# Performance work log

Measured on AMD Instinct MI355X. Metric: run time of the kernel, lower is better.

The kernel has to match this reference:

```python
import jax, jax.numpy as jnp
import numpy as np

N_NODES = 50000
N_EDGES = 500000
D_IN, D_HID = 128, 256


def _add_self_loops(edge_index, n):
    loop = jnp.arange(n, dtype=edge_index.dtype)
    src = jnp.concatenate([edge_index[0], loop])
    dst = jnp.concatenate([edge_index[1], loop])
    return src, dst


def _gcn_layer(x, W, b, src, dst, dinv_sqrt, n):
    # x: [N, d_in] -> h: [N, d_out]
    h = x @ W
    # symmetric normalization D^{-1/2} (A+I) D^{-1/2}
    norm = dinv_sqrt[src] * dinv_sqrt[dst]          # [E+N]
    msg = h[src] * norm[:, None]                    # gather + scale
    agg = jax.ops.segment_sum(msg, dst, num_segments=n)  # scatter-add
    return agg + b


def setup_inputs() -> dict:
    key = jax.random.key(0)
    ks = jax.random.split(key, 8)
    x = jax.random.normal(ks[0], (N_NODES, D_IN), dtype=jnp.float32)
    edge_index = jax.random.randint(ks[1], (2, N_EDGES), 0, N_NODES, dtype=jnp.int64 if jax.config.read('jax_enable_x64') else jnp.int32)
    s = lambda fan_in: 1.0 / np.sqrt(fan_in)
    W1 = jax.random.uniform(ks[2], (D_IN, D_HID), jnp.float32, -s(D_IN), s(D_IN))
    b1 = jnp.zeros((D_HID,), jnp.float32)
    W2 = jax.random.uniform(ks[3], (D_HID, D_HID), jnp.float32, -s(D_HID), s(D_HID))
    b2 = jnp.zeros((D_HID,), jnp.float32)
    W3 = jax.random.uniform(ks[4], (D_HID, D_HID), jnp.float32, -s(D_HID), s(D_HID))
    b3 = jnp.zeros((D_HID,), jnp.float32)
    return {"x": x, "edge_index": edge_index, "W1": W1, "b1": b1,
            "W2": W2, "b2": b2, "W3": W3, "b3": b3}


def reference(x, edge_index, W1, b1, W2, b2, W3, b3):
    n = x.shape[0]
    src, dst = _add_self_loops(edge_index, n)
    # degree includes self loops (edge weight 1), as in torch_geometric GCNConv
    deg = jax.ops.segment_sum(jnp.ones_like(dst, dtype=x.dtype), dst, num_segments=n)
    dinv_sqrt = jnp.where(deg > 0, jax.lax.rsqrt(jnp.maximum(deg, 1e-12)), 0.0)
    h = jax.nn.relu(_gcn_layer(x, W1, b1, src, dst, dinv_sqrt, n))
    h = jax.nn.relu(_gcn_layer(h, W2, b2, src, dst, dinv_sqrt, n))
    h = _gcn_layer(h, W3, b3, src, dst, dinv_sqrt, n)
    return h
```

## Files before the change

### kernel.cpp

```cpp
#include <hip/hip_runtime.h>

#define NNODES 50000
#define NEDGES 500000
#define DIN 128
#define DHID 256
#define MPAD 50048
#define NI4 12500
#define NSB 49

typedef unsigned short u16;
typedef __attribute__((ext_vector_type(8))) _Float16 half8;
typedef __attribute__((ext_vector_type(4))) float f32x4;

__device__ __forceinline__ u16 f2h(float f) {
  union { _Float16 h; u16 u; } v; v.h = (_Float16)f; return v.u;
}
__device__ __forceinline__ float h2f(unsigned int u) {
  union { _Float16 h; u16 u; } v; v.u = (u16)u; return (float)v.h;
}

__global__ void k_zero_i32(int* __restrict__ p, int n) {
  int i = blockIdx.x * blockDim.x + threadIdx.x;
  if (i < n) p[i] = 0;
}

__global__ void k_hist(const int* __restrict__ dst, int* __restrict__ deg, int e) {
  int i = blockIdx.x * blockDim.x + threadIdx.x;
  if (i < e) atomicAdd(&deg[dst[i]], 1);
}

__global__ __launch_bounds__(256) void k_blocksum(const int* __restrict__ deg,
                                                  int* __restrict__ partials) {
  __shared__ int red[256];
  int tid = threadIdx.x;
  int t4 = blockIdx.x * 256 + tid;
  int sum = 0;
  if (t4 < NI4) {
    int4 v = ((const int4*)deg)[t4];
    sum = v.x + v.y + v.z + v.w;
  }
  red[tid] = sum;
  __syncthreads();
  for (int off = 128; off > 0; off >>= 1) {
    if (tid < off) red[tid] += red[tid + off];
    __syncthreads();
  }
  if (tid == 0) partials[blockIdx.x] = red[0];
}

__global__ __launch_bounds__(256) void k_scan2(int* __restrict__ deg,
                                               const int* __restrict__ partials,
                                               int* __restrict__ row_ptr,
                                               float* __restrict__ dinv) {
  __shared__ int sdata[256];
  __shared__ int sprefix;
  int tid = threadIdx.x, bid = blockIdx.x;
  int t4 = bid * 256 + tid;
  int4 v = make_int4(0, 0, 0, 0);
  if (t4 < NI4) v = ((const int4*)deg)[t4];
  int tsum = v.x + v.y + v.z + v.w;
  sdata[tid] = tsum;
  if (tid == 0) {
    int pre = 0;
    for (int b = 0; b < bid; ++b) pre += partials[b];
    sprefix = pre;
  }
  __syncthreads();
  for (int off = 1; off < 256; off <<= 1) {
    int val = (tid >= off) ? sdata[tid - off] : 0;
    __syncthreads();
    sdata[tid] += val;
    __syncthreads();
  }
  if (t4 < NI4) {
    int run = sdata[tid] - tsum + sprefix;
    int base = t4 * 4;
    float4 dv;
    dv.x = rsqrtf((float)v.x + 1.0f);
    dv.y = rsqrtf((float)v.y + 1.0f);
    dv.z = rsqrtf((float)v.z + 1.0f);
    dv.w = rsqrtf((float)v.w + 1.0f);
    *(float4*)(dinv + base) = dv;
    row_ptr[base + 0] = run; run += v.x;
    row_ptr[base + 1] = run; run += v.y;
    row_ptr[base + 2] = run; run += v.z;
    row_ptr[base + 3] = run; run += v.w;
    if (base + 4 == NNODES) row_ptr[NNODES] = run;
    ((int4*)deg)[t4] = make_int4(0, 0, 0, 0);
  }
}

__global__ void k_fill(const int* __restrict__ src, const int* __restrict__ dst,
                       const float* __restrict__ dinv, const int* __restrict__ row_ptr,
                       int* __restrict__ cursor, int* __restrict__ csr_src,
                       float* __restrict__ csr_nrm, int e) {
  int i = blockIdx.x * blockDim.x + threadIdx.x;
  if (i < e) {
    int d = dst[i], s = src[i];
    int pos = row_ptr[d] + atomicAdd(&cursor[d], 1);
    csr_src[pos] = s;
    csr_nrm[pos] = dinv[s] * dinv[d];
  }
}

__global__ void k_prep(const float* __restrict__ x, u16* __restrict__ xh, int total4,
                       const float* __restrict__ W1f, u16* __restrict__ P1,
                       const float* __restrict__ W2f, u16* __restrict__ P2,
                       const float* __restrict__ W3f, u16* __restrict__ P3) {
  int i = blockIdx.x * blockDim.x + threadIdx.x;
  if (i < total4) {
    float4 v = ((const float4*)x)[i];
    ushort4 o;
    o.x = f2h(v.x); o.y = f2h(v.y); o.z = f2h(v.z); o.w = f2h(v.w);
    ((ushort4*)xh)[i] = o;
  }
  const int s1 = DIN * 256, s2 = s1 + DHID * 256, s3 = s2 + DHID * 256;
  if (i < s3) {
    const float* W; u16* P; int li;
    if (i < s1)      { W = W1f; P = P1; li = i; }
    else if (i < s2) { W = W2f; P = P2; li = i - s1; }
    else             { W = W3f; P = P3; li = i - s2; }
    int k = li >> 8, n = li & 255;
    int t = k >> 5, q = (k >> 3) & 3, j = k & 7;
    int c = n >> 4, m = n & 15;
    int f = (c * 64 + q * 16 + m) * 8 + j;
    float w = W[li] * 256.0f;
    u16 hi = f2h(w);
    u16 lo = f2h(w - h2f(hi));
    P[(size_t)t * 16384 + f] = hi;
    P[(size_t)t * 16384 + 8192 + f] = lo;
  }
}

template<int K, int EPI>
__global__ __launch_bounds__(256, 6) void k_fused(const u16* __restrict__ hf,
                                                  const float* __restrict__ dinv,
                                                  const int* __restrict__ row_ptr,
                                                  const int* __restrict__ csr_src,
                                                  const float* __restrict__ csr_nrm,
                                                  const u16* __restrict__ Bpk,
                                                  const float* __restrict__ bias,
                                                  u16* __restrict__ hf16,
                                                  float* __restrict__ outf) {
  __shared__ __align__(16) u16 As[32 * K];

  {
    constexpr int GL = K / 8;
    constexpr int NGRP = 256 / GL;
    constexpr int RPG = 32 / NGRP;
    const int gg = threadIdx.x / GL;
    const int sub = threadIdx.x % GL;
    const int coff = sub * 8;
    const int nbase = blockIdx.x * 32;

    for (int k = 0; k < RPG; ++k) {
      const int row = gg + k * NGRP;
      const int node = nbase + row;
      float acc[8];
      if (node < NNODES) {
        float di = dinv[node];
        float s2 = di * di;
        {
          half8 v = *(const half8*)(hf + (size_t)node * K + coff);
#pragma unroll
          for (int j = 0; j < 8; ++j) acc[j] = s2 * (float)v[j];
        }
        const int p0 = row_ptr[node];
        const int p1 = row_ptr[node + 1];
        for (int e = p0; e < p1; e += 4) {
          int idx[4]; float w[4];
#pragma unroll
          for (int q = 0; q < 4; ++q) {
            int ii = (e + q < p1) ? e + q : p1 - 1;
            idx[q] = csr_src[ii];
            w[q] = (e + q < p1) ? csr_nrm[ii] : 0.0f;
          }
          half8 v[4];
#pragma unroll
          for (int q = 0; q < 4; ++q)
            v[q] = *(const half8*)(hf + (size_t)idx[q] * K + coff);
#pragma unroll
          for (int q = 0; q < 4; ++q)
#pragma unroll
            for (int j = 0; j < 8; ++j)
              acc[j] = fmaf(w[q], (float)v[q][j], acc[j]);
        }
      } else {
#pragma unroll
        for (int j = 0; j < 8; ++j) acc[j] = 0.0f;
      }
      const int wc = coff ^ ((row & 7) << 3);
      uint4 o;
      o.x = (unsigned)f2h(acc[0]) | ((unsigned)f2h(acc[1]) << 16);
      o.y = (unsigned)f2h(acc[2]) | ((unsigned)f2h(acc[3]) << 16);
      o.z = (unsigned)f2h(acc[4]) | ((unsigned)f2h(acc[5]) << 16);
      o.w = (unsigned)f2h(acc[6]) | ((unsigned)f2h(acc[7]) << 16);
      *(uint4*)&As[row * K + wc] = o;
    }
  }

  __syncthreads();

  const int lane = threadIdx.x & 63;
  const int wave = threadIdx.x >> 6;
  const int rw = wave & 1, cw = wave >> 1;
  const int m0 = blockIdx.x * 32 + rw * 16;
  const int lr = rw * 16 + (lane & 15);
  const int acoff = (lane >> 4) * 8;

  f32x4 acc0[8];
#pragma unroll
  for (int c = 0; c < 8; ++c) acc0[c] = {0.f, 0.f, 0.f, 0.f};

  for (int t = 0; t < K / 32; ++t) {
    const int ac = acoff + t * 32;
    half8 a0 = *(const half8*)&As[lr * K + (ac ^ ((lr & 7) << 3))];
    const u16* bt = Bpk + (size_t)t * 16384 + ((size_t)cw * 8 * 64 + lane) * 8;
#pragma unroll
    for (int c = 0; c < 8; ++c) {
      const u16* fb = bt + c * 512;
      half8 bh = *(const half8*)fb;
      half8 bl = *(const half8*)(fb + 8192);
      acc0[c] = __builtin_amdgcn_mfma_f32_16x16x32_f16(a0, bh, acc0[c], 0, 0, 0);
      acc0[c] = __builtin_amdgcn_mfma_f32_16x16x32_f16(a0, bl, acc0[c], 0, 0, 0);
    }
  }

  const int cbase = lane & 15;
  const int r0 = m0 + ((lane >> 4) * 4);
  const float sc = 1.0f / 256.0f;
#pragma unroll
  for (int c = 0; c < 8; ++c) {
    int col = (cw * 8 + c) * 16 + cbase;
    float bv = bias[col];
#pragma unroll
    for (int r = 0; r < 4; ++r) {
      float v0 = fmaf(acc0[c][r], sc, bv);
      if (EPI == 0) {
        v0 = fmaxf(v0, 0.f);
        hf16[(size_t)(r0 + r) * 256 + col] = f2h(v0);
      } else {
        if (r0 + r < NNODES) outf[(size_t)(r0 + r) * 256 + col] = v0;
      }
    }
  }
}

extern "C" void kernel_launch(void* const* d_in, const int* in_sizes, int n_in,
                              void* d_out, int out_size, void* d_ws, size_t ws_size,
                              hipStream_t stream) {
  const float* x  = (const float*)d_in[0];
  const int*   ei = (const int*)d_in[1];
  const float* W1 = (const float*)d_in[2];
  const float* b1 = (const float*)d_in[3];
  const float* W2 = (const float*)d_in[4];
  const float* b2 = (const float*)d_in[5];
  const float* W3 = (const float*)d_in[6];
  const float* b3 = (const float*)d_in[7];
  float* out = (float*)d_out;
  (void)in_sizes; (void)n_in; (void)out_size; (void)ws_size;

  char* ws = (char*)d_ws;
  size_t off = 0;
  auto alloc = [&](size_t bytes) -> void* {
    void* p = (void*)(ws + off);
    off += (bytes + 255) & ~(size_t)255;
    return p;
  };
  float* dinv    = (float*)alloc((size_t)NNODES * 4);
  int*   deg     = (int*)alloc((size_t)NNODES * 4);
  int*   row_ptr = (int*)alloc((size_t)(NNODES + 1) * 4);
  int*   partials= (int*)alloc((size_t)NSB * 4);
  int*   csr_src = (int*)alloc((size_t)NEDGES * 4);
  float* csr_nrm = (float*)alloc((size_t)NEDGES * 4);
  u16*   xh      = (u16*)alloc((size_t)NNODES * DIN * 2);
  u16*   hbufA   = (u16*)alloc((size_t)MPAD * 256 * 2);
  u16*   hbufB   = (u16*)alloc((size_t)MPAD * 256 * 2);
  u16*   W1pk    = (u16*)alloc((size_t)(DIN / 32) * 16384 * 2);
  u16*   W2pk    = (u16*)alloc((size_t)(DHID / 32) * 16384 * 2);
  u16*   W3pk    = (u16*)alloc((size_t)(DHID / 32) * 16384 * 2);

  const int* e_src = ei;
  const int* e_dst = ei + NEDGES;

  const int tb = 256;
  k_zero_i32<<<(NNODES + tb - 1) / tb, tb, 0, stream>>>(deg, NNODES);
  k_hist<<<(NEDGES + tb - 1) / tb, tb, 0, stream>>>(e_dst, deg, NEDGES);
  k_blocksum<<<NSB, 256, 0, stream>>>(deg, partials);
  k_scan2<<<NSB, 256, 0, stream>>>(deg, partials, row_ptr, dinv);
  k_fill<<<(NEDGES + tb - 1) / tb, tb, 0, stream>>>(e_src, e_dst, dinv, row_ptr, deg,
                                                    csr_src, csr_nrm, NEDGES);

  int x4 = NNODES * DIN / 4;
  k_prep<<<(x4 + tb - 1) / tb, tb, 0, stream>>>(x, xh, x4,
                                                W1, W1pk, W2, W2pk, W3, W3pk);

  const int gblocks = (NNODES + 31) / 32;

  k_fused<DIN, 0><<<gblocks, 256, 0, stream>>>(xh, dinv, row_ptr, csr_src, csr_nrm,
                                               W1pk, b1, hbufA, nullptr);
  k_fused<DHID, 0><<<gblocks, 256, 0, stream>>>(hbufA, dinv, row_ptr, csr_src, csr_nrm,
                                                W2pk, b2, hbufB, nullptr);
  k_fused<DHID, 1><<<gblocks, 256, 0, stream>>>(hbufB, dinv, row_ptr, csr_src, csr_nrm,
                                                W3pk, b3, nullptr, out);
}
```

Measured before the change: 329.7 us.

## Warp-specialize fused GCN kernel: producer waves gather while consumer waves run MFMA

Each block now handles two 32-row tiles, with a double-buffered LDS A tile. Two producer waves do the sparse gather-aggregate into one buffer while two consumer waves run the MFMA GEMM over all 256 output columns on the other buffer. The grid drops to 782 blocks and launch bounds drop to 3 blocks per SIMD unit to leave room for the larger accumulator. The aim is to overlap the memory-bound gather with tensor-core work. In exchange, each phase has half the waves, the first produce and last consume are not overlapped, and LDS and register pressure rise.

```diff
diff --git a/kernel.cpp b/kernel.cpp
--- a/kernel.cpp
+++ b/kernel.cpp
@@ -7,6 +7,7 @@
 #define MPAD 50048
 #define NI4 12500
 #define NSB 49
+#define GRID 782
 
 typedef unsigned short u16;
 typedef __attribute__((ext_vector_type(8))) _Float16 half8;
@@ -133,7 +134,7 @@
 }
 
 template<int K, int EPI>
-__global__ __launch_bounds__(256, 6) void k_fused(const u16* __restrict__ hf,
+__global__ __launch_bounds__(256, 3) void k_fused(const u16* __restrict__ hf,
                                                   const float* __restrict__ dinv,
                                                   const int* __restrict__ row_ptr,
                                                   const int* __restrict__ csr_src,
@@ -142,16 +143,20 @@
                                                   const float* __restrict__ bias,
                                                   u16* __restrict__ hf16,
                                                   float* __restrict__ outf) {
-  __shared__ __align__(16) u16 As[32 * K];
-
-  {
+  __shared__ __align__(16) u16 As[2][32 * K];
+
+  const int lane = threadIdx.x & 63;
+  const int wave = threadIdx.x >> 6;
+
+  auto produce = [&](int t, int buf) {
     constexpr int GL = K / 8;
-    constexpr int NGRP = 256 / GL;
+    constexpr int NGRP = 128 / GL;
     constexpr int RPG = 32 / NGRP;
-    const int gg = threadIdx.x / GL;
-    const int sub = threadIdx.x % GL;
+    const int pid = threadIdx.x;
+    const int gg = pid / GL;
+    const int sub = pid % GL;
     const int coff = sub * 8;
-    const int nbase = blockIdx.x * 32;
+    const int nbase = t * 32;
 
     for (int k = 0; k < RPG; ++k) {
       const int row = gg + k * NGRP;
@@ -195,55 +200,63 @@
       o.y = (unsigned)f2h(acc[2]) | ((unsigned)f2h(acc[3]) << 16);
       o.z = (unsigned)f2h(acc[4]) | ((unsigned)f2h(acc[5]) << 16);
       o.w = (unsigned)f2h(acc[6]) | ((unsigned)f2h(acc[7]) << 16);
-      *(uint4*)&As[row * K + wc] = o;
+      *(uint4*)&As[buf][row * K + wc] = o;
     }
-  }
-
-  __syncthreads();
-
-  const int lane = threadIdx.x & 63;
-  const int wave = threadIdx.x >> 6;
-  const int rw = wave & 1, cw = wave >> 1;
-  const int m0 = blockIdx.x * 32 + rw * 16;
-  const int lr = rw * 16 + (lane & 15);
-  const int acoff = (lane >> 4) * 8;
-
-  f32x4 acc0[8];
-#pragma unroll
-  for (int c = 0; c < 8; ++c) acc0[c] = {0.f, 0.f, 0.f, 0.f};
-
-  for (int t = 0; t < K / 32; ++t) {
-    const int ac = acoff + t * 32;
-    half8 a0 = *(const half8*)&As[lr * K + (ac ^ ((lr & 7) << 3))];
-    const u16* bt = Bpk + (size_t)t * 16384 + ((size_t)cw * 8 * 64 + lane) * 8;
-#pragma unroll
-    for (int c = 0; c < 8; ++c) {
-      const u16* fb = bt + c * 512;
-      half8 bh = *(const half8*)fb;
-      half8 bl = *(const half8*)(fb + 8192);
-      acc0[c] = __builtin_amdgcn_mfma_f32_16x16x32_f16(a0, bh, acc0[c], 0, 0, 0);
-      acc0[c] = __builtin_amdgcn_mfma_f32_16x16x32_f16(a0, bl, acc0[c], 0, 0, 0);
-    }
-  }
-
-  const int cbase = lane & 15;
-  const int r0 = m0 + ((lane >> 4) * 4);
-  const float sc = 1.0f / 256.0f;
-#pragma unroll
-  for (int c = 0; c < 8; ++c) {
-    int col = (cw * 8 + c) * 16 + cbase;
-    float bv = bias[col];
-#pragma unroll
-    for (int r = 0; r < 4; ++r) {
-      float v0 = fmaf(acc0[c][r], sc, bv);
-      if (EPI == 0) {
-        v0 = fmaxf(v0, 0.f);
-        hf16[(size_t)(r0 + r) * 256 + col] = f2h(v0);
-      } else {
-        if (r0 + r < NNODES) outf[(size_t)(r0 + r) * 256 + col] = v0;
+  };
+
+  auto consume = [&](int t, int buf) {
+    const int rw = wave - 2;
+    const int m0 = t * 32 + rw * 16;
+    const int lr = rw * 16 + (lane & 15);
+    const int acoff = (lane >> 4) * 8;
+
+    f32x4 acc0[16];
+#pragma unroll
+    for (int c = 0; c < 16; ++c) acc0[c] = {0.f, 0.f, 0.f, 0.f};
+
+    for (int tt = 0; tt < K / 32; ++tt) {
+      const int ac = acoff + tt * 32;
+      half8 a0 = *(const half8*)&As[buf][lr * K + (ac ^ ((lr & 7) << 3))];
+      const u16* bt = Bpk + (size_t)tt * 16384 + (size_t)lane * 8;
+#pragma unroll
+      for (int c = 0; c < 16; ++c) {
+        const u16* fb = bt + c * 512;
+        half8 bh = *(const half8*)fb;
+        half8 bl = *(const half8*)(fb + 8192);
+        acc0[c] = __builtin_amdgcn_mfma_f32_16x16x32_f16(a0, bh, acc0[c], 0, 0, 0);
+        acc0[c] = __builtin_amdgcn_mfma_f32_16x16x32_f16(a0, bl, acc0[c], 0, 0, 0);
       }
     }
-  }
+
+    const int cbase = lane & 15;
+    const int r0 = m0 + ((lane >> 4) * 4);
+    const float sc = 1.0f / 256.0f;
+#pragma unroll
+    for (int c = 0; c < 16; ++c) {
+      int col = c * 16 + cbase;
+      float bv = bias[col];
+#pragma unroll
+      for (int r = 0; r < 4; ++r) {
+        float v0 = fmaf(acc0[c][r], sc, bv);
+        if (EPI == 0) {
+          v0 = fmaxf(v0, 0.f);
+          hf16[(size_t)(r0 + r) * 256 + col] = f2h(v0);
+        } else {
+          if (r0 + r < NNODES) outf[(size_t)(r0 + r) * 256 + col] = v0;
+        }
+      }
+    }
+  };
+
+  const int t0 = blockIdx.x;
+  const int t1 = blockIdx.x + GRID;
+
+  if (wave < 2) produce(t0, 0);
+  __syncthreads();
+  if (wave < 2) produce(t1, 1);
+  else          consume(t0, 0);
+  __syncthreads();
+  if (wave >= 2) consume(t1, 1);
 }
 
 extern "C" void kernel_launch(void* const* d_in, const int* in_sizes, int n_in,
@@ -295,12 +308,10 @@
   k_prep<<<(x4 + tb - 1) / tb, tb, 0, stream>>>(x, xh, x4,
                                                 W1, W1pk, W2, W2pk, W3, W3pk);
 
-  const int gblocks = (NNODES + 31) / 32;
-
-  k_fused<DIN, 0><<<gblocks, 256, 0, stream>>>(xh, dinv, row_ptr, csr_src, csr_nrm,
-                                               W1pk, b1, hbufA, nullptr);
-  k_fused<DHID, 0><<<gblocks, 256, 0, stream>>>(hbufA, dinv, row_ptr, csr_src, csr_nrm,
-                                                W2pk, b2, hbufB, nullptr);
-  k_fused<DHID, 1><<<gblocks, 256, 0, stream>>>(hbufB, dinv, row_ptr, csr_src, csr_nrm,
-                                                W3pk, b3, nullptr, out);
-}
+  k_fused<DIN, 0><<<GRID, 256, 0, stream>>>(xh, dinv, row_ptr, csr_src, csr_nrm,
+                                            W1pk, b1, hbufA, nullptr);
+  k_fused<DHID, 0><<<GRID, 256, 0, stream>>>(hbufA, dinv, row_ptr, csr_src, csr_nrm,
+                                             W2pk, b2, hbufB, nullptr);
+  k_fused<DHID, 1><<<GRID, 256, 0, stream>>>(hbufB, dinv, row_ptr, csr_src, csr_nrm,
+                                             W3pk, b3, nullptr, out);
+}
```

New measurement: 472.0 us. +43.1%, slower.

## Balance aggregation rows dynamically and reshape MFMA wave tiling to 32x64

Applied to the files above, without the earlier changes.

The gather/aggregation phase now hands out the block's 32 rows through a shared-memory atomic counter instead of a static row assignment. Thread groups that finish short neighbor lists can pick up more rows, which evens out load imbalance from varying node degrees. The GEMM phase changes each wave from 16 rows × 128 columns to 32 rows × 64 columns. This halves how often each wave loads the packed B fragments from global memory, in exchange for an extra A read from LDS. It adds per-row atomics and shuffles, plus a barrier to initialise the counter.

```diff
diff --git a/kernel.cpp b/kernel.cpp
--- a/kernel.cpp
+++ b/kernel.cpp
@@ -143,18 +143,26 @@
                                                   u16* __restrict__ hf16,
                                                   float* __restrict__ outf) {
   __shared__ __align__(16) u16 As[32 * K];
+  __shared__ int nextrow;
+
+  const int lane = threadIdx.x & 63;
+  const int wave = threadIdx.x >> 6;
+
+  if (threadIdx.x == 0) nextrow = 0;
+  __syncthreads();
 
   {
     constexpr int GL = K / 8;
-    constexpr int NGRP = 256 / GL;
-    constexpr int RPG = 32 / NGRP;
-    const int gg = threadIdx.x / GL;
     const int sub = threadIdx.x % GL;
+    const int gbase = lane - (lane % GL);
     const int coff = sub * 8;
     const int nbase = blockIdx.x * 32;
 
-    for (int k = 0; k < RPG; ++k) {
-      const int row = gg + k * NGRP;
+    for (;;) {
+      int row;
+      if (sub == 0) row = atomicAdd(&nextrow, 1);
+      row = __shfl(row, gbase);
+      if (row >= 32) break;
       const int node = nbase + row;
       float acc[8];
       if (node < NNODES) {
@@ -201,46 +209,54 @@
 
   __syncthreads();
 
-  const int lane = threadIdx.x & 63;
-  const int wave = threadIdx.x >> 6;
-  const int rw = wave & 1, cw = wave >> 1;
-  const int m0 = blockIdx.x * 32 + rw * 16;
-  const int lr = rw * 16 + (lane & 15);
+  const int cb = wave * 4;
+  const int lr0 = lane & 15;
+  const int lr1 = 16 + lr0;
   const int acoff = (lane >> 4) * 8;
 
-  f32x4 acc0[8];
-#pragma unroll
-  for (int c = 0; c < 8; ++c) acc0[c] = {0.f, 0.f, 0.f, 0.f};
+  f32x4 acc0[4], acc1[4];
+#pragma unroll
+  for (int c = 0; c < 4; ++c) {
+    acc0[c] = {0.f, 0.f, 0.f, 0.f};
+    acc1[c] = {0.f, 0.f, 0.f, 0.f};
+  }
 
   for (int t = 0; t < K / 32; ++t) {
     const int ac = acoff + t * 32;
-    half8 a0 = *(const half8*)&As[lr * K + (ac ^ ((lr & 7) << 3))];
-    const u16* bt = Bpk + (size_t)t * 16384 + ((size_t)cw * 8 * 64 + lane) * 8;
-#pragma unroll
-    for (int c = 0; c < 8; ++c) {
+    half8 a0 = *(const half8*)&As[lr0 * K + (ac ^ ((lr0 & 7) << 3))];
+    half8 a1 = *(const half8*)&As[lr1 * K + (ac ^ ((lr1 & 7) << 3))];
+    const u16* bt = Bpk + (size_t)t * 16384 + ((size_t)cb * 64 + lane) * 8;
+#pragma unroll
+    for (int c = 0; c < 4; ++c) {
       const u16* fb = bt + c * 512;
       half8 bh = *(const half8*)fb;
       half8 bl = *(const half8*)(fb + 8192);
       acc0[c] = __builtin_amdgcn_mfma_f32_16x16x32_f16(a0, bh, acc0[c], 0, 0, 0);
       acc0[c] = __builtin_amdgcn_mfma_f32_16x16x32_f16(a0, bl, acc0[c], 0, 0, 0);
+      acc1[c] = __builtin_amdgcn_mfma_f32_16x16x32_f16(a1, bh, acc1[c], 0, 0, 0);
+      acc1[c] = __builtin_amdgcn_mfma_f32_16x16x32_f16(a1, bl, acc1[c], 0, 0, 0);
     }
   }
 
   const int cbase = lane & 15;
-  const int r0 = m0 + ((lane >> 4) * 4);
+  const int r0 = blockIdx.x * 32 + ((lane >> 4) * 4);
   const float sc = 1.0f / 256.0f;
 #pragma unroll
-  for (int c = 0; c < 8; ++c) {
-    int col = (cw * 8 + c) * 16 + cbase;
+  for (int c = 0; c < 4; ++c) {
+    int col = (cb + c) * 16 + cbase;
     float bv = bias[col];
 #pragma unroll
     for (int r = 0; r < 4; ++r) {
       float v0 = fmaf(acc0[c][r], sc, bv);
+      float v1 = fmaf(acc1[c][r], sc, bv);
       if (EPI == 0) {
         v0 = fmaxf(v0, 0.f);
+        v1 = fmaxf(v1, 0.f);
         hf16[(size_t)(r0 + r) * 256 + col] = f2h(v0);
+        hf16[(size_t)(r0 + 16 + r) * 256 + col] = f2h(v1);
       } else {
         if (r0 + r < NNODES) outf[(size_t)(r0 + r) * 256 + col] = v0;
+        if (r0 + 16 + r < NNODES) outf[(size_t)(r0 + 16 + r) * 256 + col] = v1;
       }
     }
   }
```

After: 305.8 us. -7.3%, faster.
